# Optimization experiments

Hardware: AMD Instinct MI355X
Metric: run time of the kernel (lower is better)

## Reference

```python
import jax, jax.numpy as jnp
import numpy as np

F = 32        # nFilters
OPS = 5       # numOfOps (len(ratio))
CIN = 32      # in_planes of each filter's conv
N, H, W = 16, 128, 128
EPS = 1e-5    # BatchNorm2d default eps
RATIO = [0.3125, 0.3125, 0.1875, 0.125, 0.0625]


def setup_inputs() -> dict:
    key = jax.random.key(0)
    k1, k2 = jax.random.split(key, 2)
    x = jax.random.normal(k1, (N, CIN, H, W), jnp.float32)
    # each filter holds OPS weight variants (one per quantization op); 1 output channel each
    W_all = jax.random.normal(k2, (F, OPS, CIN, 3, 3), jnp.float32) * 0.05
    gamma = jnp.ones((F,), jnp.float32)
    beta = jnp.zeros((F,), jnp.float32)
    # setFiltersRatio: assign op index i to int(ratio[i]*F) consecutive filters
    counts = [int(r * F) for r in RATIO]
    counts[-1] = F - sum(counts[:-1])
    op_idx = jnp.asarray(np.repeat(np.arange(OPS), counts), jnp.int32)  # [F]
    return {"x": x, "W_all": W_all, "gamma": gamma, "beta": beta, "op_idx": op_idx}


def reference(x, W_all, gamma, beta, op_idx):
    # per-filter selection of the active op's conv weight (irregular gather)
    Wsel = W_all[jnp.arange(W_all.shape[0]), op_idx]  # [F, CIN, 3, 3]
    # all per-filter 1-out-channel convs of the same x == one grouped conv to F channels
    out1 = jax.lax.conv_general_dilated(
        x, Wsel, window_strides=(1, 1), padding="SAME",
        dimension_numbers=("NCHW", "OIHW", "NCHW"))  # [N, F, H, W]
    # BatchNorm2d in training mode: batch statistics over (N, H, W) per channel
    mean = out1.mean(axis=(0, 2, 3), keepdims=True)
    var = ((out1 - mean) ** 2).mean(axis=(0, 2, 3), keepdims=True)
    out1 = (out1 - mean) * jax.lax.rsqrt(var + EPS)
    out1 = out1 * gamma[None, :, None, None] + beta[None, :, None, None]
    # op[1] per filter: (quantized) ReLU activation — same math for every op variant
    return jax.nn.relu(out1)
```

## Files before the change

### kernel.cpp

```cpp
#include <hip/hip_runtime.h>

#define NB   16
#define CINC 32
#define HH   128
#define WWD  128
#define FF   32
#define OPSN 5
#define EPSV 1e-5f

#define WS_PARTIAL_FOFF 64
#define WS_WFRAG_BOFF   262400
#define WS_XT_BOFF      280832
#define WS_NEED         (280832 + (size_t)16*130*130*32*2)

typedef __attribute__((ext_vector_type(8))) short bf16x8;
typedef __attribute__((ext_vector_type(4))) float f32x4;

__device__ __forceinline__ unsigned short f2bf(float f) {
    unsigned u = __builtin_bit_cast(unsigned, f);
    u += 0x7FFFu + ((u >> 16) & 1u);
    return (unsigned short)(u >> 16);
}
__device__ __forceinline__ unsigned pack2(float lo, float hi) {
    return (unsigned)f2bf(lo) | ((unsigned)f2bf(hi) << 16);
}

__global__ __launch_bounds__(256) void transform_kernel(
    const float* __restrict__ x, const float* __restrict__ Wall,
    const int* __restrict__ opidx, unsigned short* __restrict__ xt,
    unsigned short* __restrict__ wfrag)
{
    __shared__ float lds[128 * 35];
    const int bid = blockIdx.x;
    const int tid = threadIdx.x;

    if (bid == NB * 130) {
        for (int idx = tid; idx < 9216; idx += 256) {
            int frag = idx >> 9;
            int lane = (idx >> 3) & 63;
            int j    = idx & 7;
            int s = frag >> 1, m = frag & 1;
            int kh = s / 3, kw = s - 3 * kh;
            int f = m * 16 + (lane & 15);
            int c = ((lane >> 4) << 3) + j;
            float v = Wall[((size_t)(f * OPSN + opidx[f]) * 288) + c * 9 + kh * 3 + kw];
            wfrag[idx] = f2bf(v);
        }
        return;
    }

    const int idx = bid >> 3;
    const int n   = (bid & 7) * 2 + (idx / 130);
    const int hp  = idx % 130;

    unsigned short* rowp = xt + (size_t)(n * 130 + hp) * 130 * 32;
    uint4 zz = make_uint4(0, 0, 0, 0);

    if (hp == 0 || hp == 129) {
        for (int c = tid; c < 520; c += 256) ((uint4*)rowp)[c] = zz;
        return;
    }

    const int h = hp - 1;
    const float* xr = x + ((size_t)n * CINC * HH + h) * WWD;
    const int c  = tid >> 3;
    const int wq = tid & 7;
#pragma unroll
    for (int it = 0; it < 4; ++it) {
        int w4 = wq + it * 8;
        float4 v = ((const float4*)(xr + (size_t)c * (HH * WWD)))[w4];
        int w = w4 * 4;
        lds[(w + 0) * 35 + c] = v.x;
        lds[(w + 1) * 35 + c] = v.y;
        lds[(w + 2) * 35 + c] = v.z;
        lds[(w + 3) * 35 + c] = v.w;
    }
    __syncthreads();
    for (int cc = tid; cc < 512; cc += 256) {
        int p = cc >> 2, k = cc & 3;
        const float* s = &lds[p * 35 + k * 8];
        uint4 o;
        o.x = pack2(s[0], s[1]); o.y = pack2(s[2], s[3]);
        o.z = pack2(s[4], s[5]); o.w = pack2(s[6], s[7]);
        ((uint4*)rowp)[4 + cc] = o;
    }
    if (tid < 4)       ((uint4*)rowp)[tid] = zz;
    else if (tid < 8)  ((uint4*)rowp)[129 * 4 + tid - 4] = zz;
}

__global__ __launch_bounds__(256) void conv_stats_kernel(
    const unsigned short* __restrict__ xt,
    const unsigned short* __restrict__ wfrag,
    float* __restrict__ partial)
{
    __shared__ float red[4][64];
    const int bid  = blockIdx.x;
    const int tid  = threadIdx.x;
    const int n    = (bid & 7) * 2 + ((bid >> 3) & 1);
    const int rest = bid >> 4;
    const int h0   = (rest & 31) * 4;
    const int wh   = rest >> 5;
    const int lane = tid & 63;
    const int wv   = tid >> 6;
    const int w0   = wh * 64 + wv * 16;
    const int l15  = lane & 15, lhi = lane >> 4;

    bf16x8 wfr[18];
#pragma unroll
    for (int i = 0; i < 18; ++i)
        wfr[i] = *(const bf16x8*)(wfrag + (i * 64 + lane) * 8);

    const unsigned short* xbase = xt + (size_t)n * 130 * 130 * 32;
    const int laneoff = l15 * 32 + lhi * 8;

    float s8[8], q8[8];
#pragma unroll
    for (int j = 0; j < 8; ++j) { s8[j] = 0.f; q8[j] = 0.f; }

    for (int h = h0; h < h0 + 4; ++h) {
        f32x4 acc0 = {0.f, 0.f, 0.f, 0.f};
        f32x4 acc1 = {0.f, 0.f, 0.f, 0.f};
#pragma unroll
        for (int kh = 0; kh < 3; ++kh) {
            const unsigned short* rp = xbase + ((size_t)(h + kh) * 130 + w0) * 32 + laneoff;
#pragma unroll
            for (int kw = 0; kw < 3; ++kw) {
                bf16x8 b = *(const bf16x8*)(rp + kw * 32);
                int s = kh * 3 + kw;
                acc0 = __builtin_amdgcn_mfma_f32_16x16x32_bf16(wfr[2*s],   b, acc0, 0, 0, 0);
                acc1 = __builtin_amdgcn_mfma_f32_16x16x32_bf16(wfr[2*s+1], b, acc1, 0, 0, 0);
            }
        }
#pragma unroll
        for (int r = 0; r < 4; ++r) {
            float v0 = acc0[r], v1 = acc1[r];
            s8[r]     += v0;  q8[r]     += v0 * v0;
            s8[4 + r] += v1;  q8[4 + r] += v1 * v1;
        }
    }

#pragma unroll
    for (int m = 1; m < 16; m <<= 1) {
#pragma unroll
        for (int j = 0; j < 8; ++j) {
            s8[j] += __shfl_xor(s8[j], m, 64);
            q8[j] += __shfl_xor(q8[j], m, 64);
        }
    }
    if (l15 == 0) {
#pragma unroll
        for (int j = 0; j < 8; ++j) {
            int f = (j < 4) ? (lhi * 4 + j) : (16 + lhi * 4 + (j - 4));
            red[wv][f]      = s8[j];
            red[wv][32 + f] = q8[j];
        }
    }
    __syncthreads();
    if (tid < 64)
        partial[(size_t)bid * 64 + tid] =
            red[0][tid] + red[1][tid] + red[2][tid] + red[3][tid];
}

__global__ __launch_bounds__(256) void stats2_kernel(
    const float* __restrict__ partial, const float* __restrict__ gamma,
    const float* __restrict__ beta, float* __restrict__ bnp)
{
    __shared__ float rs[256], rq[256];
    const int f = blockIdx.x;
    const int tid = threadIdx.x;
    float s = 0.f, q = 0.f;
#pragma unroll
    for (int k = 0; k < 4; ++k) {
        const float* p = partial + (size_t)(tid * 4 + k) * 64;
        s += p[f];
        q += p[32 + f];
    }
    rs[tid] = s; rq[tid] = q;
    __syncthreads();
    for (int st = 128; st > 0; st >>= 1) {
        if (tid < st) { rs[tid] += rs[tid + st]; rq[tid] += rq[tid + st]; }
        __syncthreads();
    }
    if (tid == 0) {
        float cnt = (float)(NB * HH * WWD);
        float mean = rs[0] / cnt;
        float var  = rq[0] / cnt - mean * mean;
        float sc = gamma[f] * rsqrtf(var + EPSV);
        bnp[f]      = sc;
        bnp[FF + f] = beta[f] - mean * sc;
    }
}

__global__ __launch_bounds__(256) void conv_apply_kernel(
    const unsigned short* __restrict__ xt,
    const unsigned short* __restrict__ wfrag,
    const float* __restrict__ bnp, float* __restrict__ out)
{
    __shared__ float bns[64];
    const int bid  = blockIdx.x;
    const int tid  = threadIdx.x;
    if (tid < 64) bns[tid] = bnp[tid];

    const int n    = (bid & 7) * 2 + ((bid >> 3) & 1);
    const int rest = bid >> 4;
    const int h0   = (rest & 31) * 4;
    const int wh   = rest >> 5;
    const int lane = tid & 63;
    const int wv   = tid >> 6;
    const int w0   = wh * 64 + wv * 16;
    const int l15  = lane & 15, lhi = lane >> 4;

    bf16x8 wfr[18];
#pragma unroll
    for (int i = 0; i < 18; ++i)
        wfr[i] = *(const bf16x8*)(wfrag + (i * 64 + lane) * 8);

    const unsigned short* xbase = xt + (size_t)n * 130 * 130 * 32;
    const int laneoff = l15 * 32 + lhi * 8;

    __syncthreads();
    float sc0[4], sh0[4], sc1[4], sh1[4];
#pragma unroll
    for (int r = 0; r < 4; ++r) {
        int f0 = lhi * 4 + r, f1 = 16 + lhi * 4 + r;
        sc0[r] = bns[f0]; sh0[r] = bns[32 + f0];
        sc1[r] = bns[f1]; sh1[r] = bns[32 + f1];
    }

    for (int h = h0; h < h0 + 4; ++h) {
        f32x4 acc0 = {0.f, 0.f, 0.f, 0.f};
        f32x4 acc1 = {0.f, 0.f, 0.f, 0.f};
#pragma unroll
        for (int kh = 0; kh < 3; ++kh) {
            const unsigned short* rp = xbase + ((size_t)(h + kh) * 130 + w0) * 32 + laneoff;
#pragma unroll
            for (int kw = 0; kw < 3; ++kw) {
                bf16x8 b = *(const bf16x8*)(rp + kw * 32);
                int s = kh * 3 + kw;
                acc0 = __builtin_amdgcn_mfma_f32_16x16x32_bf16(wfr[2*s],   b, acc0, 0, 0, 0);
                acc1 = __builtin_amdgcn_mfma_f32_16x16x32_bf16(wfr[2*s+1], b, acc1, 0, 0, 0);
            }
        }
        float* ob = out + (size_t)(n * FF + lhi * 4) * (HH * WWD) + h * WWD + w0 + l15;
#pragma unroll
        for (int r = 0; r < 4; ++r) {
            ob[(size_t)r * (HH * WWD)] =
                fmaxf(fmaf(acc0[r], sc0[r], sh0[r]), 0.f);
            ob[(size_t)r * (HH * WWD) + 16 * (HH * WWD)] =
                fmaxf(fmaf(acc1[r], sc1[r], sh1[r]), 0.f);
        }
    }
}

__global__ __launch_bounds__(256) void conv_kernel(
    const float* __restrict__ x, const float* __restrict__ Wall,
    const int* __restrict__ opidx, float* __restrict__ out)
{
    __shared__ float wlds[FF * 289];
    __shared__ float xlds[8 * 3 * 132];
    const int tid = threadIdx.x;
    const int h = blockIdx.x;
    const int n = blockIdx.y;
    for (int i = tid; i < FF * 288; i += 256) {
        int f = i / 288;
        int r = i - f * 288;
        int op = opidx[f];
        wlds[f * 289 + r] = Wall[(f * OPSN + op) * 288 + r];
    }
    const int f = tid & 31;
    const int wg = tid >> 5;
    const int w0 = wg << 4;
    float acc[16];
#pragma unroll
    for (int i = 0; i < 16; ++i) acc[i] = 0.f;
    const float* xn = x + (size_t)n * CINC * HH * WWD;
    for (int cc = 0; cc < 4; ++cc) {
        __syncthreads();
        for (int i = tid; i < 8 * 3 * 132; i += 256) {
            int c8 = i / (3 * 132);
            int rem = i - c8 * (3 * 132);
            int r = rem / 132;
            int wp = rem - r * 132;
            int hin = h + r - 1;
            int win = wp - 1;
            float v = 0.f;
            if ((unsigned)hin < HH && (unsigned)win < WWD)
                v = xn[((cc * 8 + c8) * HH + hin) * WWD + win];
            xlds[i] = v;
        }
        __syncthreads();
#pragma unroll
        for (int c8 = 0; c8 < 8; ++c8) {
            const int c = cc * 8 + c8;
            float wv[9];
#pragma unroll
            for (int k = 0; k < 9; ++k) wv[k] = wlds[f * 289 + c * 9 + k];
#pragma unroll
            for (int kh = 0; kh < 3; ++kh) {
                float xr[20];
                const float4* p = (const float4*)&xlds[(c8 * 3 + kh) * 132 + w0];
#pragma unroll
                for (int j = 0; j < 5; ++j) {
                    float4 v = p[j];
                    xr[j * 4 + 0] = v.x; xr[j * 4 + 1] = v.y;
                    xr[j * 4 + 2] = v.z; xr[j * 4 + 3] = v.w;
                }
#pragma unroll
                for (int kw = 0; kw < 3; ++kw) {
                    float wgt = wv[kh * 3 + kw];
#pragma unroll
                    for (int i = 0; i < 16; ++i)
                        acc[i] = fmaf(xr[i + kw], wgt, acc[i]);
                }
            }
        }
    }
    float* op_ = out + (((size_t)(n * FF + f) * HH + h) * WWD + w0);
#pragma unroll
    for (int j = 0; j < 4; ++j)
        ((float4*)op_)[j] = make_float4(acc[j * 4], acc[j * 4 + 1],
                                        acc[j * 4 + 2], acc[j * 4 + 3]);
}

__global__ __launch_bounds__(256) void stats_kernel(
    const float* __restrict__ out, const float* __restrict__ gamma,
    const float* __restrict__ beta, float* __restrict__ ws)
{
    __shared__ float ssum[256], ssq[256];
    const int f = blockIdx.x;
    const int tid = threadIdx.x;
    float s = 0.f, q = 0.f;
    for (int n = 0; n < NB; ++n) {
        const float4* p = (const float4*)(out + (size_t)(n * FF + f) * HH * WWD);
        for (int i = tid; i < HH * WWD / 4; i += 256) {
            float4 v = p[i];
            s += v.x + v.y + v.z + v.w;
            q += v.x * v.x + v.y * v.y + v.z * v.z + v.w * v.w;
        }
    }
    ssum[tid] = s; ssq[tid] = q;
    __syncthreads();
    for (int st = 128; st > 0; st >>= 1) {
        if (tid < st) { ssum[tid] += ssum[tid + st]; ssq[tid] += ssq[tid + st]; }
        __syncthreads();
    }
    if (tid == 0) {
        float cnt = (float)(NB * HH * WWD);
        float mean = ssum[0] / cnt;
        float var = ssq[0] / cnt - mean * mean;
        float sc = gamma[f] * rsqrtf(var + EPSV);
        ws[f] = sc;
        ws[FF + f] = beta[f] - mean * sc;
    }
}

__global__ __launch_bounds__(256) void apply_kernel(
    float* __restrict__ out, const float* __restrict__ bnp)
{
    const int total4 = NB * FF * HH * WWD / 4;
    for (int i = blockIdx.x * 256 + threadIdx.x; i < total4; i += gridDim.x * 256) {
        int f = (i >> 12) & 31;
        float sc = bnp[f], sh = bnp[FF + f];
        float4 v = ((const float4*)out)[i];
        v.x = fmaxf(fmaf(v.x, sc, sh), 0.f);
        v.y = fmaxf(fmaf(v.y, sc, sh), 0.f);
        v.z = fmaxf(fmaf(v.z, sc, sh), 0.f);
        v.w = fmaxf(fmaf(v.w, sc, sh), 0.f);
        ((float4*)out)[i] = v;
    }
}

extern "C" void kernel_launch(void* const* d_in, const int* in_sizes, int n_in,
                              void* d_out, int out_size, void* d_ws, size_t ws_size,
                              hipStream_t stream) {
    const float* x     = (const float*)d_in[0];
    const float* Wall  = (const float*)d_in[1];
    const float* gamma = (const float*)d_in[2];
    const float* beta  = (const float*)d_in[3];
    const int*   opidx = (const int*)d_in[4];
    float* out = (float*)d_out;
    float* ws  = (float*)d_ws;

    if (ws_size >= WS_NEED) {
        float*          bnp     = ws;
        float*          partial = ws + WS_PARTIAL_FOFF;
        unsigned short* wfrag   = (unsigned short*)((char*)d_ws + WS_WFRAG_BOFF);
        unsigned short* xt      = (unsigned short*)((char*)d_ws + WS_XT_BOFF);

        transform_kernel<<<NB * 130 + 1, 256, 0, stream>>>(x, Wall, opidx, xt, wfrag);
        conv_stats_kernel<<<1024, 256, 0, stream>>>(xt, wfrag, partial);
        stats2_kernel<<<FF, 256, 0, stream>>>(partial, gamma, beta, bnp);
        conv_apply_kernel<<<1024, 256, 0, stream>>>(xt, wfrag, bnp, out);
    } else {
        dim3 gridc(HH, NB);
        conv_kernel<<<gridc, 256, 0, stream>>>(x, Wall, opidx, out);
        stats_kernel<<<FF, 256, 0, stream>>>(out, gamma, beta, ws);
        apply_kernel<<<2048, 256, 0, stream>>>(out, ws);
    }
}
```

Before: 46.45 us.

## Reuse loaded input rows across four output rows with explicit sliding-window pipeline

Restructures the conv loops in the stats and apply kernels so each padded input row is loaded once and fed to up to three output-row accumulators. Input rows are software-pipelined with double-buffered register sets, which cuts global loads from 36 to 18 per wave. The change also adds nontemporal loads for x in the transform and nontemporal stores for the output. It needs more accumulator registers, which may lower occupancy.

```diff
diff --git a/kernel.cpp b/kernel.cpp
--- a/kernel.cpp
+++ b/kernel.cpp
@@ -15,6 +15,7 @@
 
 typedef __attribute__((ext_vector_type(8))) short bf16x8;
 typedef __attribute__((ext_vector_type(4))) float f32x4;
+typedef __attribute__((ext_vector_type(4))) unsigned int u32x4;
 
 __device__ __forceinline__ unsigned short f2bf(float f) {
     unsigned u = __builtin_bit_cast(unsigned, f);
@@ -68,7 +69,8 @@
 #pragma unroll
     for (int it = 0; it < 4; ++it) {
         int w4 = wq + it * 8;
-        float4 v = ((const float4*)(xr + (size_t)c * (HH * WWD)))[w4];
+        f32x4 v = __builtin_nontemporal_load(
+            (const f32x4*)(xr + (size_t)c * (HH * WWD)) + w4);
         int w = w4 * 4;
         lds[(w + 0) * 35 + c] = v.x;
         lds[(w + 1) * 35 + c] = v.y;
@@ -87,6 +89,61 @@
     if (tid < 4)       ((uint4*)rowp)[tid] = zz;
     else if (tid < 8)  ((uint4*)rowp)[129 * 4 + tid - 4] = zz;
 }
+
+#define LOADROW(f0, f1, f2, R)                                                  \
+    {                                                                           \
+        const unsigned short* rp =                                              \
+            xbase + ((size_t)(R) * 130 + w0) * 32 + laneoff;                    \
+        f0 = *(const bf16x8*)(rp);                                              \
+        f1 = *(const bf16x8*)(rp + 32);                                         \
+        f2 = *(const bf16x8*)(rp + 64);                                         \
+    }
+
+#define MROW(f0, f1, f2, aA, aB, kh)                                            \
+    {                                                                           \
+        aA = __builtin_amdgcn_mfma_f32_16x16x32_bf16(wfr[2*((kh)*3+0)],   f0, aA, 0,0,0); \
+        aB = __builtin_amdgcn_mfma_f32_16x16x32_bf16(wfr[2*((kh)*3+0)+1], f0, aB, 0,0,0); \
+        aA = __builtin_amdgcn_mfma_f32_16x16x32_bf16(wfr[2*((kh)*3+1)],   f1, aA, 0,0,0); \
+        aB = __builtin_amdgcn_mfma_f32_16x16x32_bf16(wfr[2*((kh)*3+1)+1], f1, aB, 0,0,0); \
+        aA = __builtin_amdgcn_mfma_f32_16x16x32_bf16(wfr[2*((kh)*3+2)],   f2, aA, 0,0,0); \
+        aB = __builtin_amdgcn_mfma_f32_16x16x32_bf16(wfr[2*((kh)*3+2)+1], f2, aB, 0,0,0); \
+    }
+
+#define CONV_PROLOGUE                                                           \
+    bf16x8 wfr[18];                                                             \
+    _Pragma("unroll")                                                           \
+    for (int i = 0; i < 18; ++i)                                                \
+        wfr[i] = *(const bf16x8*)(wfrag + (i * 64 + lane) * 8);                 \
+    const unsigned short* xbase = xt + (size_t)n * 130 * 130 * 32;              \
+    const int laneoff = l15 * 32 + lhi * 8;                                     \
+    f32x4 zz4 = {0.f, 0.f, 0.f, 0.f};                                           \
+    f32x4 a0A = zz4, a0B = zz4, a1A = zz4, a1B = zz4;                           \
+    f32x4 a2A = zz4, a2B = zz4, a3A = zz4, a3B = zz4;                           \
+    bf16x8 c0, c1, c2, n0, n1, n2;                                              \
+    LOADROW(c0, c1, c2, h0);                                                    \
+    LOADROW(n0, n1, n2, h0 + 1);
+
+#define CONV_BODY(FIN)                                                          \
+    MROW(c0, c1, c2, a0A, a0B, 0);                                              \
+    LOADROW(c0, c1, c2, h0 + 2);                                                \
+    MROW(n0, n1, n2, a0A, a0B, 1);                                              \
+    MROW(n0, n1, n2, a1A, a1B, 0);                                              \
+    LOADROW(n0, n1, n2, h0 + 3);                                                \
+    MROW(c0, c1, c2, a0A, a0B, 2);                                              \
+    MROW(c0, c1, c2, a1A, a1B, 1);                                              \
+    MROW(c0, c1, c2, a2A, a2B, 0);                                              \
+    FIN(a0A, a0B, 0);                                                           \
+    LOADROW(c0, c1, c2, h0 + 4);                                                \
+    MROW(n0, n1, n2, a1A, a1B, 2);                                              \
+    MROW(n0, n1, n2, a2A, a2B, 1);                                              \
+    MROW(n0, n1, n2, a3A, a3B, 0);                                              \
+    FIN(a1A, a1B, 1);                                                           \
+    LOADROW(n0, n1, n2, h0 + 5);                                                \
+    MROW(c0, c1, c2, a2A, a2B, 2);                                              \
+    MROW(c0, c1, c2, a3A, a3B, 1);                                              \
+    FIN(a2A, a2B, 2);                                                           \
+    MROW(n0, n1, n2, a3A, a3B, 2);                                              \
+    FIN(a3A, a3B, 3);
 
 __global__ __launch_bounds__(256) void conv_stats_kernel(
     const unsigned short* __restrict__ xt,
@@ -105,39 +162,23 @@
     const int w0   = wh * 64 + wv * 16;
     const int l15  = lane & 15, lhi = lane >> 4;
 
-    bf16x8 wfr[18];
-#pragma unroll
-    for (int i = 0; i < 18; ++i)
-        wfr[i] = *(const bf16x8*)(wfrag + (i * 64 + lane) * 8);
-
-    const unsigned short* xbase = xt + (size_t)n * 130 * 130 * 32;
-    const int laneoff = l15 * 32 + lhi * 8;
-
     float s8[8], q8[8];
 #pragma unroll
     for (int j = 0; j < 8; ++j) { s8[j] = 0.f; q8[j] = 0.f; }
 
-    for (int h = h0; h < h0 + 4; ++h) {
-        f32x4 acc0 = {0.f, 0.f, 0.f, 0.f};
-        f32x4 acc1 = {0.f, 0.f, 0.f, 0.f};
-#pragma unroll
-        for (int kh = 0; kh < 3; ++kh) {
-            const unsigned short* rp = xbase + ((size_t)(h + kh) * 130 + w0) * 32 + laneoff;
-#pragma unroll
-            for (int kw = 0; kw < 3; ++kw) {
-                bf16x8 b = *(const bf16x8*)(rp + kw * 32);
-                int s = kh * 3 + kw;
-                acc0 = __builtin_amdgcn_mfma_f32_16x16x32_bf16(wfr[2*s],   b, acc0, 0, 0, 0);
-                acc1 = __builtin_amdgcn_mfma_f32_16x16x32_bf16(wfr[2*s+1], b, acc1, 0, 0, 0);
-            }
-        }
-#pragma unroll
-        for (int r = 0; r < 4; ++r) {
-            float v0 = acc0[r], v1 = acc1[r];
-            s8[r]     += v0;  q8[r]     += v0 * v0;
-            s8[4 + r] += v1;  q8[4 + r] += v1 * v1;
-        }
-    }
+#define FIN_STATS(aA, aB, hh)                                                   \
+    {                                                                           \
+        _Pragma("unroll")                                                       \
+        for (int r = 0; r < 4; ++r) {                                           \
+            float v0 = aA[r], v1 = aB[r];                                       \
+            s8[r]     += v0;  q8[r]     += v0 * v0;                             \
+            s8[4 + r] += v1;  q8[4 + r] += v1 * v1;                             \
+        }                                                                       \
+    }
+
+    CONV_PROLOGUE
+    CONV_BODY(FIN_STATS)
+#undef FIN_STATS
 
 #pragma unroll
     for (int m = 1; m < 16; m <<= 1) {
@@ -210,14 +251,6 @@
     const int w0   = wh * 64 + wv * 16;
     const int l15  = lane & 15, lhi = lane >> 4;
 
-    bf16x8 wfr[18];
-#pragma unroll
-    for (int i = 0; i < 18; ++i)
-        wfr[i] = *(const bf16x8*)(wfrag + (i * 64 + lane) * 8);
-
-    const unsigned short* xbase = xt + (size_t)n * 130 * 130 * 32;
-    const int laneoff = l15 * 32 + lhi * 8;
-
     __syncthreads();
     float sc0[4], sh0[4], sc1[4], sh1[4];
 #pragma unroll
@@ -227,29 +260,24 @@
         sc1[r] = bns[f1]; sh1[r] = bns[32 + f1];
     }
 
-    for (int h = h0; h < h0 + 4; ++h) {
-        f32x4 acc0 = {0.f, 0.f, 0.f, 0.f};
-        f32x4 acc1 = {0.f, 0.f, 0.f, 0.f};
-#pragma unroll
-        for (int kh = 0; kh < 3; ++kh) {
-            const unsigned short* rp = xbase + ((size_t)(h + kh) * 130 + w0) * 32 + laneoff;
-#pragma unroll
-            for (int kw = 0; kw < 3; ++kw) {
-                bf16x8 b = *(const bf16x8*)(rp + kw * 32);
-                int s = kh * 3 + kw;
-                acc0 = __builtin_amdgcn_mfma_f32_16x16x32_bf16(wfr[2*s],   b, acc0, 0, 0, 0);
-                acc1 = __builtin_amdgcn_mfma_f32_16x16x32_bf16(wfr[2*s+1], b, acc1, 0, 0, 0);
-            }
-        }
-        float* ob = out + (size_t)(n * FF + lhi * 4) * (HH * WWD) + h * WWD + w0 + l15;
-#pragma unroll
-        for (int r = 0; r < 4; ++r) {
-            ob[(size_t)r * (HH * WWD)] =
-                fmaxf(fmaf(acc0[r], sc0[r], sh0[r]), 0.f);
-            ob[(size_t)r * (HH * WWD) + 16 * (HH * WWD)] =
-                fmaxf(fmaf(acc1[r], sc1[r], sh1[r]), 0.f);
-        }
-    }
+    float* ob = out + (size_t)(n * FF + lhi * 4) * (HH * WWD) + h0 * WWD + w0 + l15;
+
+#define FIN_APPLY(aA, aB, hh)                                                   \
+    {                                                                           \
+        _Pragma("unroll")                                                       \
+        for (int r = 0; r < 4; ++r) {                                           \
+            __builtin_nontemporal_store(                                        \
+                fmaxf(fmaf(aA[r], sc0[r], sh0[r]), 0.f),                        \
+                ob + (size_t)r * (HH * WWD) + (hh) * WWD);                      \
+            __builtin_nontemporal_store(                                        \
+                fmaxf(fmaf(aB[r], sc1[r], sh1[r]), 0.f),                        \
+                ob + (size_t)r * (HH * WWD) + 16 * (HH * WWD) + (hh) * WWD);    \
+        }                                                                       \
+    }
+
+    CONV_PROLOGUE
+    CONV_BODY(FIN_APPLY)
+#undef FIN_APPLY
 }
 
 __global__ __launch_bounds__(256) void conv_kernel(
```

New measurement: 45.71 us. Within noise of the previous version (-1.6%).
